# Kernel optimization log

Hardware: AMD Instinct MI355X
Metric: run time of the kernel (lower is better)

The kernel has to match this reference:

```python
import jax, jax.numpy as jnp
import numpy as np

HIDDEN = 2048
HEADS = 16
LN_EPS = 1e-5


def setup_inputs() -> dict:
    key = jax.random.key(0)
    ks = jax.random.split(key, 12)
    B, S, D = 4, 4096, HIDDEN
    std = 0.02
    inp = {
        "x": jax.random.normal(ks[0], (B, S, D), dtype=jnp.float32),
        "ln_g": jnp.ones((D,), dtype=jnp.float32),
        "ln_b": jnp.zeros((D,), dtype=jnp.float32),
        # weights stored as [in, out] so y = x @ W + b (equivalent to torch Linear)
        "Wq": jax.random.normal(ks[1], (D, D), dtype=jnp.float32) * std,
        "bq": jnp.zeros((D,), dtype=jnp.float32),
        "Wk": jax.random.normal(ks[2], (D, D), dtype=jnp.float32) * std,
        "bk": jnp.zeros((D,), dtype=jnp.float32),
        "Wv": jax.random.normal(ks[3], (D, D), dtype=jnp.float32) * std,
        "bv": jnp.zeros((D,), dtype=jnp.float32),
        "Wo": jax.random.normal(ks[4], (D, D), dtype=jnp.float32) * std,
        "bo": jnp.zeros((D,), dtype=jnp.float32),
    }
    return inp


def reference(x, ln_g, ln_b, Wq, bq, Wk, bk, Wv, bv, Wo, bo):
    B, S, D = x.shape
    H = HEADS
    hd = D // H
    # LayerNorm
    mu = jnp.mean(x, axis=-1, keepdims=True)
    var = jnp.mean(jnp.square(x - mu), axis=-1, keepdims=True)
    xn = (x - mu) * jax.lax.rsqrt(var + LN_EPS) * ln_g + ln_b
    # QKV projections
    q = (xn @ Wq + bq).reshape(B, S, H, hd)
    k = (xn @ Wk + bk).reshape(B, S, H, hd)
    v = (xn @ Wv + bv).reshape(B, S, H, hd)
    # Faithful to source: q @ k.transpose(-2,-1) on [B,S,H,hd] -> scores [B,S,H,H]
    # (attention mixes across heads per token; scale uses full hidden_dim)
    scores = jnp.einsum('bshd,bsgd->bshg', q, k) / jnp.sqrt(jnp.float32(D))
    weights = jax.nn.softmax(scores, axis=-1)
    context = jnp.einsum('bshg,bsgd->bshd', weights, v).reshape(B, S, D)
    out = context @ Wo + bo
    return out
```

## Files before the change

kernel.cpp:

```cpp
#include <hip/hip_runtime.h>

typedef __bf16 bf16x8 __attribute__((ext_vector_type(8)));
typedef __bf16 bf16x4 __attribute__((ext_vector_type(4)));
typedef float  f32x4  __attribute__((ext_vector_type(4)));

#define GLOAD_LDS16(g, l) \
  __builtin_amdgcn_global_load_lds((const __attribute__((address_space(1))) void*)(g), \
                                   (__attribute__((address_space(3))) void*)(l), 16, 0, 0)

__global__ __launch_bounds__(256) void wcvt_kernel(
    const float* __restrict__ W0, const float* __restrict__ W1,
    const float* __restrict__ W2, const float* __restrict__ W3,
    __bf16* __restrict__ WtBase)
{
  const float* W = (blockIdx.z == 0) ? W0 : (blockIdx.z == 1) ? W1 : (blockIdx.z == 2) ? W2 : W3;
  __bf16* dst = WtBase + (size_t)blockIdx.z * 2048 * 2048;
  __shared__ float tile[32][33];
  const int tx = threadIdx.x & 31, ty = threadIdx.x >> 5;
  const int gi = blockIdx.x * 32, gj = blockIdx.y * 32;
  #pragma unroll
  for (int r = 0; r < 32; r += 8)
    tile[ty + r][tx] = W[(size_t)(gi + ty + r) * 2048 + gj + tx];
  __syncthreads();
  #pragma unroll
  for (int r = 0; r < 32; r += 8)
    dst[(size_t)(gj + ty + r) * 2048 + gi + tx] = (__bf16)tile[tx][ty + r];
}

__global__ __launch_bounds__(256) void ln_kernel(
    const float* __restrict__ x, const float* __restrict__ gw,
    const float* __restrict__ bw, __bf16* __restrict__ xn)
{
  __shared__ float red[8];
  const size_t base = (size_t)blockIdx.x * 2048;
  const int t = threadIdx.x;
  float4 v0 = *(const float4*)(x + base + t * 4);
  float4 v1 = *(const float4*)(x + base + 1024 + t * 4);
  float sm = v0.x + v0.y + v0.z + v0.w + v1.x + v1.y + v1.z + v1.w;
  float sq = v0.x*v0.x + v0.y*v0.y + v0.z*v0.z + v0.w*v0.w
           + v1.x*v1.x + v1.y*v1.y + v1.z*v1.z + v1.w*v1.w;
  #pragma unroll
  for (int off = 32; off; off >>= 1) {
    sm += __shfl_down(sm, off);
    sq += __shfl_down(sq, off);
  }
  if ((t & 63) == 0) { red[t >> 6] = sm; red[4 + (t >> 6)] = sq; }
  __syncthreads();
  const float fs = red[0] + red[1] + red[2] + red[3];
  const float fq = red[4] + red[5] + red[6] + red[7];
  const float mu = fs * (1.f / 2048.f);
  const float var = fq * (1.f / 2048.f) - mu * mu;
  const float rs = rsqrtf(var + 1e-5f);
  float4 g0 = *(const float4*)(gw + t * 4);
  float4 g1 = *(const float4*)(gw + 1024 + t * 4);
  float4 b0 = *(const float4*)(bw + t * 4);
  float4 b1 = *(const float4*)(bw + 1024 + t * 4);
  bf16x4 o0, o1;
  o0[0] = (__bf16)((v0.x - mu) * rs * g0.x + b0.x);
  o0[1] = (__bf16)((v0.y - mu) * rs * g0.y + b0.y);
  o0[2] = (__bf16)((v0.z - mu) * rs * g0.z + b0.z);
  o0[3] = (__bf16)((v0.w - mu) * rs * g0.w + b0.w);
  o1[0] = (__bf16)((v1.x - mu) * rs * g1.x + b1.x);
  o1[1] = (__bf16)((v1.y - mu) * rs * g1.y + b1.y);
  o1[2] = (__bf16)((v1.z - mu) * rs * g1.z + b1.z);
  o1[3] = (__bf16)((v1.w - mu) * rs * g1.w + b1.w);
  *(bf16x4*)(xn + base + t * 4) = o0;
  *(bf16x4*)(xn + base + 1024 + t * 4) = o1;
}

template <int MODE>
__global__ __launch_bounds__(512, 2) void gemm256(
    const __bf16* __restrict__ A, int lda,
    const __bf16* __restrict__ WtBase,
    const float* __restrict__ b0, const float* __restrict__ b1,
    const float* __restrict__ b2, void* __restrict__ outp)
{
  __shared__ __attribute__((aligned(16))) char smem[131072];
  const int tid = threadIdx.x, lane = tid & 63, wid = tid >> 6;
  const int wm = wid >> 2, wn = wid & 3;
  const int m0 = blockIdx.x * 256;
  int which, n0;
  const __bf16* Bt;
  const float* bias;
  if (MODE == 0) {
    which = blockIdx.y >> 3;
    n0 = (blockIdx.y & 7) * 256;
    Bt = WtBase + (size_t)which * 2048 * 2048 + (size_t)n0 * 2048;
    bias = (which == 0) ? b0 : (which == 1) ? b1 : b2;
  } else {
    which = 0;
    n0 = blockIdx.y * 256;
    Bt = WtBase + (size_t)n0 * 2048;
    bias = b0;
  }

  const int srow = tid >> 3;
  const int segl = (tid & 7) ^ (srow & 7);
  const __bf16* Ag[4];
  const __bf16* Bg[4];
  #pragma unroll
  for (int g = 0; g < 4; g++) {
    Ag[g] = A  + (size_t)(m0 + g * 64 + srow) * lda  + segl * 8;
    Bg[g] = Bt + (size_t)(g * 64 + srow)      * 2048 + segl * 8;
  }
  const int ldst = __builtin_amdgcn_readfirstlane(wid * 1024);

#define STAGE_TILE(buf, kt)                                                  \
  do {                                                                       \
    const int koff_ = (kt) * 64;                                             \
    _Pragma("unroll") for (int g_ = 0; g_ < 4; g_++)                         \
      GLOAD_LDS16(Ag[g_] + koff_, smem + (buf) * 32768 + g_ * 8192 + ldst);  \
    _Pragma("unroll") for (int g_ = 0; g_ < 4; g_++)                         \
      GLOAD_LDS16(Bg[g_] + koff_, smem + 65536 + (buf) * 32768 + g_ * 8192 + ldst); \
  } while (0)

  const int fr = lane & 15, sl = lane >> 4, x78 = fr & 7;
  const int off0 = (sl ^ x78) * 16;
  const int off1 = ((4 + sl) ^ x78) * 16;
  const int abase = (wm * 128 + fr) * 128;
  const int bbase = (wn * 64 + fr) * 128;

  f32x4 acc[8][4];
  #pragma unroll
  for (int i = 0; i < 8; i++)
    #pragma unroll
    for (int j = 0; j < 4; j++) acc[i][j] = (f32x4){0.f, 0.f, 0.f, 0.f};

  STAGE_TILE(0, 0);
  const int NT = 2048 / 64;

  for (int t = 0; t < NT; t++) {
    const int c = t & 1;
    __syncthreads();
    if (t + 1 < NT) STAGE_TILE(c ^ 1, t + 1);
    const char* Ab = smem + c * 32768;
    const char* Bb = smem + 65536 + c * 32768;
    #pragma unroll
    for (int ks = 0; ks < 2; ks++) {
      const int ofk = ks ? off1 : off0;
      bf16x8 bfr[4];
      #pragma unroll
      for (int ni = 0; ni < 4; ni++)
        bfr[ni] = *(const bf16x8*)(Bb + bbase + ni * 2048 + ofk);
      #pragma unroll
      for (int mh = 0; mh < 2; mh++) {
        bf16x8 afr[4];
        #pragma unroll
        for (int i = 0; i < 4; i++)
          afr[i] = *(const bf16x8*)(Ab + abase + (mh * 4 + i) * 2048 + ofk);
        __builtin_amdgcn_s_setprio(1);
        #pragma unroll
        for (int i = 0; i < 4; i++)
          #pragma unroll
          for (int ni = 0; ni < 4; ni++)
            acc[mh * 4 + i][ni] =
                __builtin_amdgcn_mfma_f32_16x16x32_bf16(afr[i], bfr[ni], acc[mh * 4 + i][ni], 0, 0, 0);
        __builtin_amdgcn_s_setprio(0);
        if (!(ks == 1 && mh == 1)) __builtin_amdgcn_s_barrier();
      }
    }
  }
#undef STAGE_TILE

  const int colf = lane & 15, rowf = (lane >> 4) * 4;
  #pragma unroll
  for (int mi = 0; mi < 8; mi++) {
    const int rw = m0 + wm * 128 + mi * 16 + rowf;
    #pragma unroll
    for (int ni = 0; ni < 4; ni++) {
      const int cc = n0 + wn * 64 + ni * 16 + colf;
      const float bi = bias[cc];
      if (MODE == 0) {
        __bf16* qkv = (__bf16*)outp;
        #pragma unroll
        for (int j = 0; j < 4; j++)
          qkv[(size_t)(rw + j) * 6144 + (size_t)which * 2048 + cc] =
              (__bf16)(acc[mi][ni][j] + bi);
      } else {
        float* out = (float*)outp;
        #pragma unroll
        for (int j = 0; j < 4; j++)
          out[(size_t)(rw + j) * 2048 + cc] = acc[mi][ni][j] + bi;
      }
    }
  }
}

__global__ __launch_bounds__(256) void attn_kernel(__bf16* __restrict__ qkv)
{
  __shared__ __bf16 att[4 * 6144];
  __shared__ float Psh[4 * 256];
  const int tid = threadIdx.x, lane = tid & 63, w = tid >> 6;
  const size_t token = (size_t)blockIdx.x * 4 + w;
  const __bf16* src = qkv + token * 6144;
  char* ldsb = (char*)att;
  const int lbase = __builtin_amdgcn_readfirstlane(w * 12288);
  #pragma unroll
  for (int r = 0; r < 12; r++)
    GLOAD_LDS16(src + r * 512 + lane * 8, ldsb + lbase + r * 1024);
  __syncthreads();

  const __bf16* my = att + w * 6144;
  const int h = lane >> 2, gq = lane & 3;
  const __bf16* qrow = my + h * 128;
  float s[4] = {0.f, 0.f, 0.f, 0.f};
  for (int d = 0; d < 128; d += 8) {
    bf16x8 qv = *(const bf16x8*)(qrow + d);
    float qf[8];
    #pragma unroll
    for (int j = 0; j < 8; j++) qf[j] = (float)qv[j];
    #pragma unroll
    for (int i = 0; i < 4; i++) {
      bf16x8 kv = *(const bf16x8*)(my + 2048 + (gq * 4 + i) * 128 + d);
      #pragma unroll
      for (int j = 0; j < 8; j++) s[i] += qf[j] * (float)kv[j];
    }
  }
  const float scale = 0.022097086912079612f;
  #pragma unroll
  for (int i = 0; i < 4; i++) s[i] *= scale;
  float mx = fmaxf(fmaxf(s[0], s[1]), fmaxf(s[2], s[3]));
  mx = fmaxf(mx, __shfl_xor(mx, 1));
  mx = fmaxf(mx, __shfl_xor(mx, 2));
  float p[4], sum = 0.f;
  #pragma unroll
  for (int i = 0; i < 4; i++) { p[i] = __expf(s[i] - mx); sum += p[i]; }
  sum += __shfl_xor(sum, 1);
  sum += __shfl_xor(sum, 2);
  const float inv = 1.f / sum;
  #pragma unroll
  for (int i = 0; i < 4; i++) Psh[w * 256 + h * 16 + gq * 4 + i] = p[i] * inv;
  __syncthreads();

  const int h2 = lane >> 2, db = (lane & 3) * 32;
  const __bf16* vb = my + 4096;
  float acc[32];
  #pragma unroll
  for (int i = 0; i < 32; i++) acc[i] = 0.f;
  for (int g = 0; g < 16; g++) {
    const float pv = Psh[w * 256 + h2 * 16 + g];
    #pragma unroll
    for (int c = 0; c < 4; c++) {
      bf16x8 vv = *(const bf16x8*)(vb + g * 128 + db + c * 8);
      #pragma unroll
      for (int j = 0; j < 8; j++) acc[c * 8 + j] += pv * (float)vv[j];
    }
  }
  __bf16* dst = qkv + token * 6144 + h2 * 128 + db;
  #pragma unroll
  for (int c = 0; c < 4; c++) {
    bf16x8 ov;
    #pragma unroll
    for (int j = 0; j < 8; j++) ov[j] = (__bf16)acc[c * 8 + j];
    *(bf16x8*)(dst + c * 8) = ov;
  }
}

extern "C" void kernel_launch(void* const* d_in, const int* in_sizes, int n_in,
                              void* d_out, int out_size, void* d_ws, size_t ws_size,
                              hipStream_t stream)
{
  const float* x    = (const float*)d_in[0];
  const float* ln_g = (const float*)d_in[1];
  const float* ln_b = (const float*)d_in[2];
  const float* Wq   = (const float*)d_in[3];
  const float* bq   = (const float*)d_in[4];
  const float* Wk   = (const float*)d_in[5];
  const float* bk   = (const float*)d_in[6];
  const float* Wv   = (const float*)d_in[7];
  const float* bv   = (const float*)d_in[8];
  const float* Wo   = (const float*)d_in[9];
  const float* bo   = (const float*)d_in[10];
  float* out = (float*)d_out;
  const int M = in_sizes[0] / 2048;

  char* ws = (char*)d_ws;
  __bf16* Wt  = (__bf16*)ws;
  __bf16* qkv = (__bf16*)(ws + 33554432);
  __bf16* xn  = (__bf16*)d_out;

  wcvt_kernel<<<dim3(64, 64, 4), 256, 0, stream>>>(Wq, Wk, Wv, Wo, Wt);
  ln_kernel<<<M, 256, 0, stream>>>(x, ln_g, ln_b, xn);
  gemm256<0><<<dim3(M / 256, 24), 512, 0, stream>>>(xn, 2048, Wt, bq, bk, bv, (void*)qkv);
  attn_kernel<<<M / 4, 256, 0, stream>>>(qkv);
  gemm256<1><<<dim3(M / 256, 8), 512, 0, stream>>>(qkv, 6144, Wt + (size_t)3 * 2048 * 2048,
                                                   bo, nullptr, nullptr, (void*)out);
}
```

Baseline: 640.2 us.

## Restructure GEMM main loop into four-phase half-tile ping-pong with deeper prefetch

The GEMM main loop now splits each 256x256 K-tile into half-tiles of A and B and runs four MFMA phases per iteration, one per (A half, B half) quadrant. Global-to-LDS loads for later half-tiles, up to two K-steps ahead, are issued between phases and gated by explicit vmcnt waits, replacing the single per-tile syncthreads. The aim is to overlap memory traffic with MFMA work more finely and keep fewer fragments live at once. In exchange it adds more barriers per iteration and relies on hand-tuned waitcnt values and a changed row/column-to-accumulator mapping, so correctness depends on that mapping matching the unchanged epilogue.

```diff
diff --git a/kernel.cpp b/kernel.cpp
--- a/kernel.cpp
+++ b/kernel.cpp
@@ -94,73 +94,101 @@
     bias = b0;
   }
 
-  const int srow = tid >> 3;
-  const int segl = (tid & 7) ^ (srow & 7);
-  const __bf16* Ag[4];
-  const __bf16* Bg[4];
-  #pragma unroll
-  for (int g = 0; g < 4; g++) {
-    Ag[g] = A  + (size_t)(m0 + g * 64 + srow) * lda  + segl * 8;
-    Bg[g] = Bt + (size_t)(g * 64 + srow)      * 2048 + segl * 8;
-  }
+  const int lr0 = tid >> 3;
+  const int sg  = (tid & 7) ^ (lr0 & 7);
+  const __bf16* Ag0 = A + (size_t)(m0 + lr0) * lda + sg * 8;
+  const __bf16* Ag1 = A + (size_t)(m0 + 64 + lr0) * lda + sg * 8;
+  const __bf16* Bg0 = Bt + (size_t)((lr0 >> 5) * 64 + (lr0 & 31)) * 2048 + sg * 8;
+  const __bf16* Bg1 = Bt + (size_t)((lr0 >> 5) * 64 + 32 + (lr0 & 31)) * 2048 + sg * 8;
   const int ldst = __builtin_amdgcn_readfirstlane(wid * 1024);
 
-#define STAGE_TILE(buf, kt)                                                  \
-  do {                                                                       \
-    const int koff_ = (kt) * 64;                                             \
-    _Pragma("unroll") for (int g_ = 0; g_ < 4; g_++)                         \
-      GLOAD_LDS16(Ag[g_] + koff_, smem + (buf) * 32768 + g_ * 8192 + ldst);  \
-    _Pragma("unroll") for (int g_ = 0; g_ < 4; g_++)                         \
-      GLOAD_LDS16(Bg[g_] + koff_, smem + 65536 + (buf) * 32768 + g_ * 8192 + ldst); \
+#define STAGE_A(H, DBB, KT)                                                        \
+  do {                                                                             \
+    GLOAD_LDS16(Ag##H + (KT) * 64, smem + (DBB) + (H) * 16384 + ldst);             \
+    GLOAD_LDS16(Ag##H + (size_t)128 * lda + (KT) * 64,                             \
+                smem + (DBB) + (H) * 16384 + 8192 + ldst);                         \
   } while (0)
-
-  const int fr = lane & 15, sl = lane >> 4, x78 = fr & 7;
-  const int off0 = (sl ^ x78) * 16;
-  const int off1 = ((4 + sl) ^ x78) * 16;
-  const int abase = (wm * 128 + fr) * 128;
-  const int bbase = (wn * 64 + fr) * 128;
-
+#define STAGE_B(H, DBB, KT)                                                        \
+  do {                                                                             \
+    GLOAD_LDS16(Bg##H + (KT) * 64, smem + (DBB) + 32768 + (H) * 16384 + ldst);     \
+    GLOAD_LDS16(Bg##H + 262144 + (KT) * 64,                                        \
+                smem + (DBB) + 32768 + (H) * 16384 + 8192 + ldst);                 \
+  } while (0)
+
+  const int fr = lane & 15, sl = lane >> 4, x7 = fr & 7;
+  const int aoff0 = (wm * 64 + fr) * 128 + ((sl) ^ x7) * 16;
+  const int aoff1 = (wm * 64 + fr) * 128 + ((4 + sl) ^ x7) * 16;
+  const int boff0 = (wn * 32 + fr) * 128 + ((sl) ^ x7) * 16;
+  const int boff1 = (wn * 32 + fr) * 128 + ((4 + sl) ^ x7) * 16;
+
+  bf16x8 afr[4][2], bfr0[2][2], bfr1[2][2];
   f32x4 acc[8][4];
   #pragma unroll
   for (int i = 0; i < 8; i++)
     #pragma unroll
     for (int j = 0; j < 4; j++) acc[i][j] = (f32x4){0.f, 0.f, 0.f, 0.f};
 
-  STAGE_TILE(0, 0);
-  const int NT = 2048 / 64;
-
-  for (int t = 0; t < NT; t++) {
-    const int c = t & 1;
-    __syncthreads();
-    if (t + 1 < NT) STAGE_TILE(c ^ 1, t + 1);
-    const char* Ab = smem + c * 32768;
-    const char* Bb = smem + 65536 + c * 32768;
-    #pragma unroll
-    for (int ks = 0; ks < 2; ks++) {
-      const int ofk = ks ? off1 : off0;
-      bf16x8 bfr[4];
-      #pragma unroll
-      for (int ni = 0; ni < 4; ni++)
-        bfr[ni] = *(const bf16x8*)(Bb + bbase + ni * 2048 + ofk);
-      #pragma unroll
-      for (int mh = 0; mh < 2; mh++) {
-        bf16x8 afr[4];
-        #pragma unroll
-        for (int i = 0; i < 4; i++)
-          afr[i] = *(const bf16x8*)(Ab + abase + (mh * 4 + i) * 2048 + ofk);
-        __builtin_amdgcn_s_setprio(1);
-        #pragma unroll
-        for (int i = 0; i < 4; i++)
-          #pragma unroll
-          for (int ni = 0; ni < 4; ni++)
-            acc[mh * 4 + i][ni] =
-                __builtin_amdgcn_mfma_f32_16x16x32_bf16(afr[i], bfr[ni], acc[mh * 4 + i][ni], 0, 0, 0);
-        __builtin_amdgcn_s_setprio(0);
-        if (!(ks == 1 && mh == 1)) __builtin_amdgcn_s_barrier();
-      }
-    }
-  }
-#undef STAGE_TILE
+#define READ_A(MH, DB)                                                             \
+  _Pragma("unroll") for (int mi = 0; mi < 4; mi++)                                 \
+  _Pragma("unroll") for (int kk = 0; kk < 2; kk++)                                 \
+    afr[mi][kk] = *(const bf16x8*)(smem + (DB) + (MH) * 16384 +                    \
+                                   (kk ? aoff1 : aoff0) + mi * 2048);
+#define READ_B(NH, DB, DEST)                                                       \
+  _Pragma("unroll") for (int ni = 0; ni < 2; ni++)                                 \
+  _Pragma("unroll") for (int kk = 0; kk < 2; kk++)                                 \
+    DEST[ni][kk] = *(const bf16x8*)(smem + (DB) + 32768 + (NH) * 16384 +           \
+                                    (kk ? boff1 : boff0) + ni * 2048);
+#define MFMA16(MH, NH, BSET)                                                       \
+  _Pragma("unroll") for (int kk = 0; kk < 2; kk++)                                 \
+  _Pragma("unroll") for (int mi = 0; mi < 4; mi++)                                 \
+  _Pragma("unroll") for (int ni = 0; ni < 2; ni++)                                 \
+    acc[(MH) * 4 + mi][(NH) * 2 + ni] = __builtin_amdgcn_mfma_f32_16x16x32_bf16(   \
+        afr[mi][kk], BSET[ni][kk], acc[(MH) * 4 + mi][(NH) * 2 + ni], 0, 0, 0);
+#define PHASE_TAIL(MH, NH, BSET)                                                   \
+  __builtin_amdgcn_s_barrier();                                                    \
+  asm volatile("s_waitcnt lgkmcnt(0)" ::: "memory");                               \
+  __builtin_amdgcn_sched_barrier(0);                                               \
+  __builtin_amdgcn_s_setprio(1);                                                   \
+  MFMA16(MH, NH, BSET);                                                            \
+  __builtin_amdgcn_s_setprio(0);                                                   \
+  __builtin_amdgcn_s_barrier();
+
+  STAGE_A(0, 0, 0);
+  STAGE_B(0, 0, 0);
+  STAGE_A(1, 0, 0);
+  STAGE_B(1, 0, 0);
+  STAGE_A(0, 65536, 1);
+  STAGE_B(0, 65536, 1);
+  STAGE_B(1, 65536, 1);
+  __syncthreads();
+
+  const int NT = 32;
+  for (int kt = 0; kt < NT; kt++) {
+    const int db  = (kt & 1) << 16;
+    const int dbn = db ^ 65536;
+    if (kt == NT - 1) { asm volatile("s_waitcnt vmcnt(0)" ::: "memory"); }
+    else              { asm volatile("s_waitcnt vmcnt(6)" ::: "memory"); }
+    READ_A(0, db);
+    READ_B(0, db, bfr0);
+    if (kt + 1 < NT) STAGE_A(1, dbn, kt + 1);
+    PHASE_TAIL(0, 0, bfr0);
+    asm volatile("s_waitcnt vmcnt(6)" ::: "memory");
+    READ_B(1, db, bfr1);
+    if (kt + 2 < NT) STAGE_A(0, db, kt + 2);
+    PHASE_TAIL(0, 1, bfr1);
+    asm volatile("s_waitcnt vmcnt(6)" ::: "memory");
+    READ_A(1, db);
+    if (kt + 2 < NT) STAGE_B(0, db, kt + 2);
+    PHASE_TAIL(1, 1, bfr1);
+    if (kt + 2 < NT) STAGE_B(1, db, kt + 2);
+    PHASE_TAIL(1, 0, bfr0);
+  }
+#undef STAGE_A
+#undef STAGE_B
+#undef READ_A
+#undef READ_B
+#undef MFMA16
+#undef PHASE_TAIL
 
   const int colf = lane & 15, rowf = (lane >> 4) * 4;
   #pragma unroll
```

New measurement: 624.2 us. -2.5%, faster.
